# Kernel optimization log

Hardware: AMD Instinct MI355X
Metric: run time of the kernel (lower is better)

Reference implementation:

```python
import jax, jax.numpy as jnp
import numpy as np

R, F, H = 256, 1024, 256  # num_robots, num_frontiers, hidden_dim


def setup_inputs() -> dict:
    key = jax.random.key(0)
    ks = jax.random.split(key, 16)
    sc = 0.05
    return {
        "robot_features": jax.random.normal(ks[0], (R, 4), jnp.float32),
        "frontier_features": jax.random.normal(ks[1], (F, 3), jnp.float32),
        # robot encoder: Linear(4,H) -> ReLU -> Linear(H,H)
        "r_w1": jax.random.normal(ks[2], (4, H), jnp.float32) * sc,
        "r_b1": jnp.zeros((H,), jnp.float32),
        "r_w2": jax.random.normal(ks[3], (H, H), jnp.float32) * sc,
        "r_b2": jnp.zeros((H,), jnp.float32),
        # frontier encoder: Linear(3,H) -> ReLU -> Linear(H,H)
        "f_w1": jax.random.normal(ks[4], (3, H), jnp.float32) * sc,
        "f_b1": jnp.zeros((H,), jnp.float32),
        "f_w2": jax.random.normal(ks[5], (H, H), jnp.float32) * sc,
        "f_b2": jnp.zeros((H,), jnp.float32),
        # affinity predictor: Linear(2H,H) -> ReLU -> Linear(H,1)
        "a_w1": jax.random.normal(ks[6], (2 * H, H), jnp.float32) * sc,
        "a_b1": jnp.zeros((H,), jnp.float32),
        "a_w2": jax.random.normal(ks[7], (H, 1), jnp.float32) * sc,
        "a_b2": jnp.zeros((1,), jnp.float32),
    }


def reference(robot_features, frontier_features,
              r_w1, r_b1, r_w2, r_b2,
              f_w1, f_b1, f_w2, f_b2,
              a_w1, a_b1, a_w2, a_b2):
    # encoders: Linear -> ReLU -> Linear
    robot_embed = jax.nn.relu(robot_features @ r_w1 + r_b1) @ r_w2 + r_b2      # (R, H)
    frontier_embed = jax.nn.relu(frontier_features @ f_w1 + f_b1) @ f_w2 + f_b2  # (F, H)

    # Vectorized pairwise concat: split a_w1 into robot/frontier halves so we
    # never materialize the (R, F, 2H) concat explicitly.
    w1_r, w1_f = a_w1[:robot_embed.shape[1]], a_w1[robot_embed.shape[1]:]
    h = robot_embed @ w1_r  # (R, H)
    h = h[:, None, :] + (frontier_embed @ w1_f)[None, :, :] + a_b1  # (R, F, H)
    h = jax.nn.relu(h)
    affinity = (h @ a_w2)[..., 0] + a_b2[0]  # (R, F)
    return affinity
```

## Files before the change

kernel.cpp:

```cpp
#include <hip/hip_runtime.h>
#include <hip/hip_bf16.h>

#define H 256
#define R_N 256
#define F_N 1024

__global__ __launch_bounds__(256) void embed_kernel(
    const float* __restrict__ rf, const float* __restrict__ ff,
    const float* __restrict__ r_w1, const float* __restrict__ r_b1,
    const float* __restrict__ r_w2, const float* __restrict__ r_b2,
    const float* __restrict__ f_w1, const float* __restrict__ f_b1,
    const float* __restrict__ f_w2, const float* __restrict__ f_b2,
    const float* __restrict__ a_w1, const float* __restrict__ a_b1,
    float* __restrict__ u, float* __restrict__ v)
{
    const int t = threadIdx.x;
    __shared__ float a_s[4][H];
    __shared__ float e_s[4][H];

    if (blockIdx.x < 64) {
        const int r0 = blockIdx.x * 4;
        #pragma unroll
        for (int g = 0; g < 4; ++g) {
            const int r = r0 + g;
            float acc = r_b1[t];
            acc = fmaf(rf[r * 4 + 0], r_w1[0 * H + t], acc);
            acc = fmaf(rf[r * 4 + 1], r_w1[1 * H + t], acc);
            acc = fmaf(rf[r * 4 + 2], r_w1[2 * H + t], acc);
            acc = fmaf(rf[r * 4 + 3], r_w1[3 * H + t], acc);
            a_s[g][t] = fmaxf(acc, 0.0f);
        }
        __syncthreads();

        float e0 = r_b2[t], e1 = e0, e2 = e0, e3 = e0;
        #pragma unroll 8
        for (int k = 0; k < H; ++k) {
            const float w = r_w2[k * H + t];
            e0 = fmaf(a_s[0][k], w, e0);
            e1 = fmaf(a_s[1][k], w, e1);
            e2 = fmaf(a_s[2][k], w, e2);
            e3 = fmaf(a_s[3][k], w, e3);
        }
        __syncthreads();
        e_s[0][t] = e0; e_s[1][t] = e1; e_s[2][t] = e2; e_s[3][t] = e3;
        __syncthreads();

        float u0 = 0.f, u1 = 0.f, u2 = 0.f, u3 = 0.f;
        #pragma unroll 8
        for (int n = 0; n < H; ++n) {
            const float w = a_w1[n * H + t];
            u0 = fmaf(e_s[0][n], w, u0);
            u1 = fmaf(e_s[1][n], w, u1);
            u2 = fmaf(e_s[2][n], w, u2);
            u3 = fmaf(e_s[3][n], w, u3);
        }
        u[(r0 + 0) * H + t] = u0;
        u[(r0 + 1) * H + t] = u1;
        u[(r0 + 2) * H + t] = u2;
        u[(r0 + 3) * H + t] = u3;
    } else {
        const int f0 = (blockIdx.x - 64) * 4;
        #pragma unroll
        for (int g = 0; g < 4; ++g) {
            const int f = f0 + g;
            float acc = f_b1[t];
            acc = fmaf(ff[f * 3 + 0], f_w1[0 * H + t], acc);
            acc = fmaf(ff[f * 3 + 1], f_w1[1 * H + t], acc);
            acc = fmaf(ff[f * 3 + 2], f_w1[2 * H + t], acc);
            a_s[g][t] = fmaxf(acc, 0.0f);
        }
        __syncthreads();

        float e0 = f_b2[t], e1 = e0, e2 = e0, e3 = e0;
        #pragma unroll 8
        for (int k = 0; k < H; ++k) {
            const float w = f_w2[k * H + t];
            e0 = fmaf(a_s[0][k], w, e0);
            e1 = fmaf(a_s[1][k], w, e1);
            e2 = fmaf(a_s[2][k], w, e2);
            e3 = fmaf(a_s[3][k], w, e3);
        }
        __syncthreads();
        e_s[0][t] = e0; e_s[1][t] = e1; e_s[2][t] = e2; e_s[3][t] = e3;
        __syncthreads();

        const float bias = a_b1[t];
        float v0 = bias, v1 = bias, v2 = bias, v3 = bias;
        #pragma unroll 8
        for (int n = 0; n < H; ++n) {
            const float w = a_w1[(H + n) * H + t];
            v0 = fmaf(e_s[0][n], w, v0);
            v1 = fmaf(e_s[1][n], w, v1);
            v2 = fmaf(e_s[2][n], w, v2);
            v3 = fmaf(e_s[3][n], w, v3);
        }
        v[(f0 + 0) * H + t] = v0;
        v[(f0 + 1) * H + t] = v1;
        v[(f0 + 2) * H + t] = v2;
        v[(f0 + 3) * H + t] = v3;
    }
}

#define PAD 260

__global__ __launch_bounds__(256) void affinity_kernel(
    const float* __restrict__ u, const float* __restrict__ v,
    const float* __restrict__ a_w2, const float* __restrict__ a_b2,
    float* __restrict__ out)
{
    __shared__ float u_s[32][PAD];
    __shared__ float v_s[32][PAD];
    __shared__ float w_s[H];

    const int t  = threadIdx.x;
    const int r0 = (blockIdx.x >> 5) * 32;
    const int f0 = (blockIdx.x & 31) * 32;

    w_s[t] = a_w2[t];

    {
        const int rr = t >> 6;
        const int cc = (t & 63) << 2;
        #pragma unroll
        for (int i = 0; i < 8; ++i) {
            const int row = rr + i * 4;
            *(float4*)&u_s[row][cc] = *(const float4*)&u[(r0 + row) * H + cc];
            *(float4*)&v_s[row][cc] = *(const float4*)&v[(f0 + row) * H + cc];
        }
    }
    __syncthreads();

    const int fi = t & 15;
    const int ri = t >> 4;

    float acc00 = 0.f, acc01 = 0.f, acc10 = 0.f, acc11 = 0.f;
    #pragma unroll 4
    for (int k = 0; k < H; k += 4) {
        const float4 w4 = *(const float4*)&w_s[k];
        const float4 ua = *(const float4*)&u_s[ri][k];
        const float4 ub = *(const float4*)&u_s[ri + 16][k];
        const float4 va = *(const float4*)&v_s[fi][k];
        const float4 vb = *(const float4*)&v_s[fi + 16][k];

        acc00 = fmaf(fmaxf(ua.x + va.x, 0.f), w4.x, acc00);
        acc00 = fmaf(fmaxf(ua.y + va.y, 0.f), w4.y, acc00);
        acc00 = fmaf(fmaxf(ua.z + va.z, 0.f), w4.z, acc00);
        acc00 = fmaf(fmaxf(ua.w + va.w, 0.f), w4.w, acc00);

        acc01 = fmaf(fmaxf(ua.x + vb.x, 0.f), w4.x, acc01);
        acc01 = fmaf(fmaxf(ua.y + vb.y, 0.f), w4.y, acc01);
        acc01 = fmaf(fmaxf(ua.z + vb.z, 0.f), w4.z, acc01);
        acc01 = fmaf(fmaxf(ua.w + vb.w, 0.f), w4.w, acc01);

        acc10 = fmaf(fmaxf(ub.x + va.x, 0.f), w4.x, acc10);
        acc10 = fmaf(fmaxf(ub.y + va.y, 0.f), w4.y, acc10);
        acc10 = fmaf(fmaxf(ub.z + va.z, 0.f), w4.z, acc10);
        acc10 = fmaf(fmaxf(ub.w + va.w, 0.f), w4.w, acc10);

        acc11 = fmaf(fmaxf(ub.x + vb.x, 0.f), w4.x, acc11);
        acc11 = fmaf(fmaxf(ub.y + vb.y, 0.f), w4.y, acc11);
        acc11 = fmaf(fmaxf(ub.z + vb.z, 0.f), w4.z, acc11);
        acc11 = fmaf(fmaxf(ub.w + vb.w, 0.f), w4.w, acc11);
    }

    const float b = a_b2[0];
    out[(r0 + ri)      * F_N + f0 + fi]      = acc00 + b;
    out[(r0 + ri)      * F_N + f0 + fi + 16] = acc01 + b;
    out[(r0 + ri + 16) * F_N + f0 + fi]      = acc10 + b;
    out[(r0 + ri + 16) * F_N + f0 + fi + 16] = acc11 + b;
}

extern "C" void kernel_launch(void* const* d_in, const int* in_sizes, int n_in,
                              void* d_out, int out_size, void* d_ws, size_t ws_size,
                              hipStream_t stream) {
    const float* rf   = (const float*)d_in[0];
    const float* ff   = (const float*)d_in[1];
    const float* r_w1 = (const float*)d_in[2];
    const float* r_b1 = (const float*)d_in[3];
    const float* r_w2 = (const float*)d_in[4];
    const float* r_b2 = (const float*)d_in[5];
    const float* f_w1 = (const float*)d_in[6];
    const float* f_b1 = (const float*)d_in[7];
    const float* f_w2 = (const float*)d_in[8];
    const float* f_b2 = (const float*)d_in[9];
    const float* a_w1 = (const float*)d_in[10];
    const float* a_b1 = (const float*)d_in[11];
    const float* a_w2 = (const float*)d_in[12];
    const float* a_b2 = (const float*)d_in[13];

    float* u = (float*)d_ws;
    float* v = u + R_N * H;

    embed_kernel<<<320, 256, 0, stream>>>(rf, ff, r_w1, r_b1, r_w2, r_b2,
                                          f_w1, f_b1, f_w2, f_b2,
                                          a_w1, a_b1, u, v);
    affinity_kernel<<<256, 256, 0, stream>>>(u, v, a_w2, a_b2, (float*)d_out);
}
```

Baseline: 31.03 us.

## Split K across waves in embed and affinity kernels with shared-memory reduction

The embed kernel now handles 8 rows per block (160 blocks instead of 320). Each wave covers a quarter of the K dimension with float4 weight loads and an 8x4 register tile, and partial sums are reduced through shared memory. The affinity kernel moves to 512 threads with a 4-way K split and a 4x2 output tile per thread, then reduces through shared memory. The aim is to cut per-thread serial K loops and raise weight-load reuse, at the cost of extra reduction traffic, more barriers and larger shared-memory footprints.

```diff
diff --git a/kernel.cpp b/kernel.cpp
--- a/kernel.cpp
+++ b/kernel.cpp
@@ -4,6 +4,12 @@
 #define H 256
 #define R_N 256
 #define F_N 1024
+
+#define FMA4(A, s, W) \
+    A.x = fmaf((s), (W).x, A.x); \
+    A.y = fmaf((s), (W).y, A.y); \
+    A.z = fmaf((s), (W).z, A.z); \
+    A.w = fmaf((s), (W).w, A.w);
 
 __global__ __launch_bounds__(256) void embed_kernel(
     const float* __restrict__ rf, const float* __restrict__ ff,
@@ -14,160 +20,206 @@
     const float* __restrict__ a_w1, const float* __restrict__ a_b1,
     float* __restrict__ u, float* __restrict__ v)
 {
-    const int t = threadIdx.x;
-    __shared__ float a_s[4][H];
-    __shared__ float e_s[4][H];
-
-    if (blockIdx.x < 64) {
-        const int r0 = blockIdx.x * 4;
-        #pragma unroll
-        for (int g = 0; g < 4; ++g) {
-            const int r = r0 + g;
-            float acc = r_b1[t];
-            acc = fmaf(rf[r * 4 + 0], r_w1[0 * H + t], acc);
-            acc = fmaf(rf[r * 4 + 1], r_w1[1 * H + t], acc);
-            acc = fmaf(rf[r * 4 + 2], r_w1[2 * H + t], acc);
-            acc = fmaf(rf[r * 4 + 3], r_w1[3 * H + t], acc);
-            a_s[g][t] = fmaxf(acc, 0.0f);
-        }
-        __syncthreads();
-
-        float e0 = r_b2[t], e1 = e0, e2 = e0, e3 = e0;
+    const int t  = threadIdx.x;
+    const int wp = t >> 6;
+    const int c  = (t & 63) * 4;
+
+    __shared__ float aT[H][8];
+    __shared__ float red[4][8][H];
+
+    const bool robot = blockIdx.x < 32;
+    const int  g0    = robot ? blockIdx.x * 8 : (blockIdx.x - 32) * 8;
+
+    const float* __restrict__ x   = robot ? (rf + g0 * 4) : (ff + g0 * 3);
+    const int                 ind = robot ? 4 : 3;
+    const float* __restrict__ w1  = robot ? r_w1 : f_w1;
+    const float* __restrict__ b1  = robot ? r_b1 : f_b1;
+    const float* __restrict__ W2  = robot ? r_w2 : f_w2;
+    const float* __restrict__ b2  = robot ? r_b2 : f_b2;
+    const int                 k3  = robot ? 0 : H;
+    float* __restrict__       dst = robot ? u : v;
+
+    {
+        float l1[8];
+        const float bb = b1[t];
+        #pragma unroll
+        for (int g = 0; g < 8; ++g) {
+            float acc = bb;
+            for (int j = 0; j < ind; ++j)
+                acc = fmaf(x[g * ind + j], w1[j * H + t], acc);
+            l1[g] = fmaxf(acc, 0.0f);
+        }
+        *(float4*)&aT[t][0] = make_float4(l1[0], l1[1], l1[2], l1[3]);
+        *(float4*)&aT[t][4] = make_float4(l1[4], l1[5], l1[6], l1[7]);
+    }
+    __syncthreads();
+
+    {
+        float4 acc[8];
+        #pragma unroll
+        for (int g = 0; g < 8; ++g) acc[g] = make_float4(0.f, 0.f, 0.f, 0.f);
+
+        const int kbase = wp * 64;
         #pragma unroll 8
-        for (int k = 0; k < H; ++k) {
-            const float w = r_w2[k * H + t];
-            e0 = fmaf(a_s[0][k], w, e0);
-            e1 = fmaf(a_s[1][k], w, e1);
-            e2 = fmaf(a_s[2][k], w, e2);
-            e3 = fmaf(a_s[3][k], w, e3);
-        }
-        __syncthreads();
-        e_s[0][t] = e0; e_s[1][t] = e1; e_s[2][t] = e2; e_s[3][t] = e3;
-        __syncthreads();
-
-        float u0 = 0.f, u1 = 0.f, u2 = 0.f, u3 = 0.f;
+        for (int kk = 0; kk < 64; ++kk) {
+            const int k = kbase + kk;
+            const float4 w4  = *(const float4*)&W2[k * H + c];
+            const float4 alo = *(const float4*)&aT[k][0];
+            const float4 ahi = *(const float4*)&aT[k][4];
+            FMA4(acc[0], alo.x, w4); FMA4(acc[1], alo.y, w4);
+            FMA4(acc[2], alo.z, w4); FMA4(acc[3], alo.w, w4);
+            FMA4(acc[4], ahi.x, w4); FMA4(acc[5], ahi.y, w4);
+            FMA4(acc[6], ahi.z, w4); FMA4(acc[7], ahi.w, w4);
+        }
+        #pragma unroll
+        for (int g = 0; g < 8; ++g) *(float4*)&red[wp][g][c] = acc[g];
+    }
+    __syncthreads();
+
+    {
+        float e[8];
+        const float bb = b2[t];
+        #pragma unroll
+        for (int g = 0; g < 8; ++g)
+            e[g] = red[0][g][t] + red[1][g][t] + red[2][g][t] + red[3][g][t] + bb;
+        *(float4*)&aT[t][0] = make_float4(e[0], e[1], e[2], e[3]);
+        *(float4*)&aT[t][4] = make_float4(e[4], e[5], e[6], e[7]);
+    }
+    __syncthreads();
+
+    {
+        float4 acc[8];
+        #pragma unroll
+        for (int g = 0; g < 8; ++g) acc[g] = make_float4(0.f, 0.f, 0.f, 0.f);
+
+        const int kbase = wp * 64;
         #pragma unroll 8
-        for (int n = 0; n < H; ++n) {
-            const float w = a_w1[n * H + t];
-            u0 = fmaf(e_s[0][n], w, u0);
-            u1 = fmaf(e_s[1][n], w, u1);
-            u2 = fmaf(e_s[2][n], w, u2);
-            u3 = fmaf(e_s[3][n], w, u3);
-        }
-        u[(r0 + 0) * H + t] = u0;
-        u[(r0 + 1) * H + t] = u1;
-        u[(r0 + 2) * H + t] = u2;
-        u[(r0 + 3) * H + t] = u3;
-    } else {
-        const int f0 = (blockIdx.x - 64) * 4;
-        #pragma unroll
-        for (int g = 0; g < 4; ++g) {
-            const int f = f0 + g;
-            float acc = f_b1[t];
-            acc = fmaf(ff[f * 3 + 0], f_w1[0 * H + t], acc);
-            acc = fmaf(ff[f * 3 + 1], f_w1[1 * H + t], acc);
-            acc = fmaf(ff[f * 3 + 2], f_w1[2 * H + t], acc);
-            a_s[g][t] = fmaxf(acc, 0.0f);
-        }
-        __syncthreads();
-
-        float e0 = f_b2[t], e1 = e0, e2 = e0, e3 = e0;
-        #pragma unroll 8
-        for (int k = 0; k < H; ++k) {
-            const float w = f_w2[k * H + t];
-            e0 = fmaf(a_s[0][k], w, e0);
-            e1 = fmaf(a_s[1][k], w, e1);
-            e2 = fmaf(a_s[2][k], w, e2);
-            e3 = fmaf(a_s[3][k], w, e3);
-        }
-        __syncthreads();
-        e_s[0][t] = e0; e_s[1][t] = e1; e_s[2][t] = e2; e_s[3][t] = e3;
-        __syncthreads();
-
-        const float bias = a_b1[t];
-        float v0 = bias, v1 = bias, v2 = bias, v3 = bias;
-        #pragma unroll 8
-        for (int n = 0; n < H; ++n) {
-            const float w = a_w1[(H + n) * H + t];
-            v0 = fmaf(e_s[0][n], w, v0);
-            v1 = fmaf(e_s[1][n], w, v1);
-            v2 = fmaf(e_s[2][n], w, v2);
-            v3 = fmaf(e_s[3][n], w, v3);
-        }
-        v[(f0 + 0) * H + t] = v0;
-        v[(f0 + 1) * H + t] = v1;
-        v[(f0 + 2) * H + t] = v2;
-        v[(f0 + 3) * H + t] = v3;
+        for (int kk = 0; kk < 64; ++kk) {
+            const int k = kbase + kk;
+            const float4 w4  = *(const float4*)&a_w1[(k3 + k) * H + c];
+            const float4 alo = *(const float4*)&aT[k][0];
+            const float4 ahi = *(const float4*)&aT[k][4];
+            FMA4(acc[0], alo.x, w4); FMA4(acc[1], alo.y, w4);
+            FMA4(acc[2], alo.z, w4); FMA4(acc[3], alo.w, w4);
+            FMA4(acc[4], ahi.x, w4); FMA4(acc[5], ahi.y, w4);
+            FMA4(acc[6], ahi.z, w4); FMA4(acc[7], ahi.w, w4);
+        }
+        #pragma unroll
+        for (int g = 0; g < 8; ++g) *(float4*)&red[wp][g][c] = acc[g];
+    }
+    __syncthreads();
+
+    {
+        const float ab = robot ? 0.0f : a_b1[t];
+        #pragma unroll
+        for (int g = 0; g < 8; ++g) {
+            const float s = red[0][g][t] + red[1][g][t] + red[2][g][t] + red[3][g][t] + ab;
+            dst[(g0 + g) * H + t] = s;
+        }
     }
 }
 
-#define PAD 260
-
-__global__ __launch_bounds__(256) void affinity_kernel(
+#define LDP 260
+
+__global__ __launch_bounds__(512) void affinity_kernel(
     const float* __restrict__ u, const float* __restrict__ v,
     const float* __restrict__ a_w2, const float* __restrict__ a_b2,
     float* __restrict__ out)
 {
-    __shared__ float u_s[32][PAD];
-    __shared__ float v_s[32][PAD];
+    __shared__ float u_s[32][LDP];
+    __shared__ float v_s[32][LDP];
     __shared__ float w_s[H];
+    __shared__ float red[4][32][33];
 
     const int t  = threadIdx.x;
     const int r0 = (blockIdx.x >> 5) * 32;
     const int f0 = (blockIdx.x & 31) * 32;
 
-    w_s[t] = a_w2[t];
-
-    {
-        const int rr = t >> 6;
-        const int cc = (t & 63) << 2;
-        #pragma unroll
-        for (int i = 0; i < 8; ++i) {
-            const int row = rr + i * 4;
-            *(float4*)&u_s[row][cc] = *(const float4*)&u[(r0 + row) * H + cc];
-            *(float4*)&v_s[row][cc] = *(const float4*)&v[(f0 + row) * H + cc];
-        }
-    }
-    __syncthreads();
-
-    const int fi = t & 15;
-    const int ri = t >> 4;
-
-    float acc00 = 0.f, acc01 = 0.f, acc10 = 0.f, acc11 = 0.f;
+    #pragma unroll
+    for (int i = 0; i < 4; ++i) {
+        const int slot = t + i * 512;
+        const int row  = slot >> 6;
+        const int cc   = (slot & 63) * 4;
+        *(float4*)&u_s[row][cc] = *(const float4*)&u[(r0 + row) * H + cc];
+        *(float4*)&v_s[row][cc] = *(const float4*)&v[(f0 + row) * H + cc];
+    }
+    if (t < 64) *(float4*)&w_s[t * 4] = *(const float4*)&a_w2[t * 4];
+    __syncthreads();
+
+    const int kp = t >> 7;
+    const int t7 = t & 127;
+    const int ri = t7 >> 4;
+    const int fi = t7 & 15;
+    const int k0 = kp * 64;
+
+    float4 accA = make_float4(0.f, 0.f, 0.f, 0.f);
+    float4 accB = make_float4(0.f, 0.f, 0.f, 0.f);
+
     #pragma unroll 4
-    for (int k = 0; k < H; k += 4) {
+    for (int kk = 0; kk < 64; kk += 4) {
+        const int k = k0 + kk;
         const float4 w4 = *(const float4*)&w_s[k];
-        const float4 ua = *(const float4*)&u_s[ri][k];
-        const float4 ub = *(const float4*)&u_s[ri + 16][k];
+        const float4 u0 = *(const float4*)&u_s[ri][k];
+        const float4 u1 = *(const float4*)&u_s[ri +  8][k];
+        const float4 u2 = *(const float4*)&u_s[ri + 16][k];
+        const float4 u3 = *(const float4*)&u_s[ri + 24][k];
         const float4 va = *(const float4*)&v_s[fi][k];
         const float4 vb = *(const float4*)&v_s[fi + 16][k];
 
-        acc00 = fmaf(fmaxf(ua.x + va.x, 0.f), w4.x, acc00);
-        acc00 = fmaf(fmaxf(ua.y + va.y, 0.f), w4.y, acc00);
-        acc00 = fmaf(fmaxf(ua.z + va.z, 0.f), w4.z, acc00);
-        acc00 = fmaf(fmaxf(ua.w + va.w, 0.f), w4.w, acc00);
-
-        acc01 = fmaf(fmaxf(ua.x + vb.x, 0.f), w4.x, acc01);
-        acc01 = fmaf(fmaxf(ua.y + vb.y, 0.f), w4.y, acc01);
-        acc01 = fmaf(fmaxf(ua.z + vb.z, 0.f), w4.z, acc01);
-        acc01 = fmaf(fmaxf(ua.w + vb.w, 0.f), w4.w, acc01);
-
-        acc10 = fmaf(fmaxf(ub.x + va.x, 0.f), w4.x, acc10);
-        acc10 = fmaf(fmaxf(ub.y + va.y, 0.f), w4.y, acc10);
-        acc10 = fmaf(fmaxf(ub.z + va.z, 0.f), w4.z, acc10);
-        acc10 = fmaf(fmaxf(ub.w + va.w, 0.f), w4.w, acc10);
-
-        acc11 = fmaf(fmaxf(ub.x + vb.x, 0.f), w4.x, acc11);
-        acc11 = fmaf(fmaxf(ub.y + vb.y, 0.f), w4.y, acc11);
-        acc11 = fmaf(fmaxf(ub.z + vb.z, 0.f), w4.z, acc11);
-        acc11 = fmaf(fmaxf(ub.w + vb.w, 0.f), w4.w, acc11);
-    }
+        accA.x = fmaf(fmaxf(u0.x + va.x, 0.f), w4.x, accA.x);
+        accA.x = fmaf(fmaxf(u0.y + va.y, 0.f), w4.y, accA.x);
+        accA.x = fmaf(fmaxf(u0.z + va.z, 0.f), w4.z, accA.x);
+        accA.x = fmaf(fmaxf(u0.w + va.w, 0.f), w4.w, accA.x);
+        accA.y = fmaf(fmaxf(u1.x + va.x, 0.f), w4.x, accA.y);
+        accA.y = fmaf(fmaxf(u1.y + va.y, 0.f), w4.y, accA.y);
+        accA.y = fmaf(fmaxf(u1.z + va.z, 0.f), w4.z, accA.y);
+        accA.y = fmaf(fmaxf(u1.w + va.w, 0.f), w4.w, accA.y);
+        accA.z = fmaf(fmaxf(u2.x + va.x, 0.f), w4.x, accA.z);
+        accA.z = fmaf(fmaxf(u2.y + va.y, 0.f), w4.y, accA.z);
+        accA.z = fmaf(fmaxf(u2.z + va.z, 0.f), w4.z, accA.z);
+        accA.z = fmaf(fmaxf(u2.w + va.w, 0.f), w4.w, accA.z);
+        accA.w = fmaf(fmaxf(u3.x + va.x, 0.f), w4.x, accA.w);
+        accA.w = fmaf(fmaxf(u3.y + va.y, 0.f), w4.y, accA.w);
+        accA.w = fmaf(fmaxf(u3.z + va.z, 0.f), w4.z, accA.w);
+        accA.w = fmaf(fmaxf(u3.w + va.w, 0.f), w4.w, accA.w);
+
+        accB.x = fmaf(fmaxf(u0.x + vb.x, 0.f), w4.x, accB.x);
+        accB.x = fmaf(fmaxf(u0.y + vb.y, 0.f), w4.y, accB.x);
+        accB.x = fmaf(fmaxf(u0.z + vb.z, 0.f), w4.z, accB.x);
+        accB.x = fmaf(fmaxf(u0.w + vb.w, 0.f), w4.w, accB.x);
+        accB.y = fmaf(fmaxf(u1.x + vb.x, 0.f), w4.x, accB.y);
+        accB.y = fmaf(fmaxf(u1.y + vb.y, 0.f), w4.y, accB.y);
+        accB.y = fmaf(fmaxf(u1.z + vb.z, 0.f), w4.z, accB.y);
+        accB.y = fmaf(fmaxf(u1.w + vb.w, 0.f), w4.w, accB.y);
+        accB.z = fmaf(fmaxf(u2.x + vb.x, 0.f), w4.x, accB.z);
+        accB.z = fmaf(fmaxf(u2.y + vb.y, 0.f), w4.y, accB.z);
+        accB.z = fmaf(fmaxf(u2.z + vb.z, 0.f), w4.z, accB.z);
+        accB.z = fmaf(fmaxf(u2.w + vb.w, 0.f), w4.w, accB.z);
+        accB.w = fmaf(fmaxf(u3.x + vb.x, 0.f), w4.x, accB.w);
+        accB.w = fmaf(fmaxf(u3.y + vb.y, 0.f), w4.y, accB.w);
+        accB.w = fmaf(fmaxf(u3.z + vb.z, 0.f), w4.z, accB.w);
+        accB.w = fmaf(fmaxf(u3.w + vb.w, 0.f), w4.w, accB.w);
+    }
+
+    red[kp][ri]     [fi]      = accA.x;
+    red[kp][ri +  8][fi]      = accA.y;
+    red[kp][ri + 16][fi]      = accA.z;
+    red[kp][ri + 24][fi]      = accA.w;
+    red[kp][ri]     [fi + 16] = accB.x;
+    red[kp][ri +  8][fi + 16] = accB.y;
+    red[kp][ri + 16][fi + 16] = accB.z;
+    red[kp][ri + 24][fi + 16] = accB.w;
+    __syncthreads();
 
     const float b = a_b2[0];
-    out[(r0 + ri)      * F_N + f0 + fi]      = acc00 + b;
-    out[(r0 + ri)      * F_N + f0 + fi + 16] = acc01 + b;
-    out[(r0 + ri + 16) * F_N + f0 + fi]      = acc10 + b;
-    out[(r0 + ri + 16) * F_N + f0 + fi + 16] = acc11 + b;
+    #pragma unroll
+    for (int j = 0; j < 2; ++j) {
+        const int o = t + j * 512;
+        const int r = o >> 5;
+        const int f = o & 31;
+        const float s = red[0][r][f] + red[1][r][f] + red[2][r][f] + red[3][r][f] + b;
+        out[(r0 + r) * F_N + f0 + f] = s;
+    }
 }
 
 extern "C" void kernel_launch(void* const* d_in, const int* in_sizes, int n_in,
@@ -191,8 +243,8 @@
     float* u = (float*)d_ws;
     float* v = u + R_N * H;
 
-    embed_kernel<<<320, 256, 0, stream>>>(rf, ff, r_w1, r_b1, r_w2, r_b2,
+    embed_kernel<<<160, 256, 0, stream>>>(rf, ff, r_w1, r_b1, r_w2, r_b2,
                                           f_w1, f_b1, f_w2, f_b2,
                                           a_w1, a_b1, u, v);
-    affinity_kernel<<<256, 256, 0, stream>>>(u, v, a_w2, a_b2, (float*)d_out);
+    affinity_kernel<<<256, 512, 0, stream>>>(u, v, a_w2, a_b2, (float*)d_out);
 }
```

Measured after the change: 35.24 us. +13.6%, slower.

## Split affinity K-reduction across four thread groups with 4x2 register tiles

Applied to the files above, without the earlier changes.

The affinity kernel now runs 512 threads per block. Each group of 128 threads handles one quarter of the hidden dimension and computes a 4x2 output micro-tile, and the four partial sums are combined through a shared-memory reduction buffer. The aim is to double the active waves per block, reuse each loaded v vector across more rows, and coalesce the output stores. The cost is an extra shared-memory buffer, an extra barrier, and a reduction pass before the write.

```diff
diff --git a/kernel.cpp b/kernel.cpp
--- a/kernel.cpp
+++ b/kernel.cpp
@@ -101,73 +101,107 @@
     }
 }
 
-#define PAD 260
-
-__global__ __launch_bounds__(256) void affinity_kernel(
+#define LDP 260
+
+__global__ __launch_bounds__(512) void affinity_kernel(
     const float* __restrict__ u, const float* __restrict__ v,
     const float* __restrict__ a_w2, const float* __restrict__ a_b2,
     float* __restrict__ out)
 {
-    __shared__ float u_s[32][PAD];
-    __shared__ float v_s[32][PAD];
+    __shared__ float u_s[32][LDP];
+    __shared__ float v_s[32][LDP];
     __shared__ float w_s[H];
+    __shared__ float red[4][32][33];
 
     const int t  = threadIdx.x;
     const int r0 = (blockIdx.x >> 5) * 32;
     const int f0 = (blockIdx.x & 31) * 32;
 
-    w_s[t] = a_w2[t];
-
-    {
-        const int rr = t >> 6;
-        const int cc = (t & 63) << 2;
-        #pragma unroll
-        for (int i = 0; i < 8; ++i) {
-            const int row = rr + i * 4;
-            *(float4*)&u_s[row][cc] = *(const float4*)&u[(r0 + row) * H + cc];
-            *(float4*)&v_s[row][cc] = *(const float4*)&v[(f0 + row) * H + cc];
-        }
-    }
+    #pragma unroll
+    for (int i = 0; i < 4; ++i) {
+        const int slot = t + i * 512;
+        const int row  = slot >> 6;
+        const int cc   = (slot & 63) * 4;
+        *(float4*)&u_s[row][cc] = *(const float4*)&u[(r0 + row) * H + cc];
+        *(float4*)&v_s[row][cc] = *(const float4*)&v[(f0 + row) * H + cc];
+    }
+    if (t < 64) *(float4*)&w_s[t * 4] = *(const float4*)&a_w2[t * 4];
     __syncthreads();
 
-    const int fi = t & 15;
-    const int ri = t >> 4;
-
-    float acc00 = 0.f, acc01 = 0.f, acc10 = 0.f, acc11 = 0.f;
+    const int kp = t >> 7;
+    const int t7 = t & 127;
+    const int ri = t7 >> 4;
+    const int fi = t7 & 15;
+    const int k0 = kp * 64;
+
+    float4 accA = make_float4(0.f, 0.f, 0.f, 0.f);
+    float4 accB = make_float4(0.f, 0.f, 0.f, 0.f);
+
     #pragma unroll 4
-    for (int k = 0; k < H; k += 4) {
+    for (int kk = 0; kk < 64; kk += 4) {
+        const int k = k0 + kk;
         const float4 w4 = *(const float4*)&w_s[k];
-        const float4 ua = *(const float4*)&u_s[ri][k];
-        const float4 ub = *(const float4*)&u_s[ri + 16][k];
+        const float4 u0 = *(const float4*)&u_s[ri][k];
+        const float4 u1 = *(const float4*)&u_s[ri +  8][k];
+        const float4 u2 = *(const float4*)&u_s[ri + 16][k];
+        const float4 u3 = *(const float4*)&u_s[ri + 24][k];
         const float4 va = *(const float4*)&v_s[fi][k];
         const float4 vb = *(const float4*)&v_s[fi + 16][k];
 
-        acc00 = fmaf(fmaxf(ua.x + va.x, 0.f), w4.x, acc00);
-        acc00 = fmaf(fmaxf(ua.y + va.y, 0.f), w4.y, acc00);
-        acc00 = fmaf(fmaxf(ua.z + va.z, 0.f), w4.z, acc00);
-        acc00 = fmaf(fmaxf(ua.w + va.w, 0.f), w4.w, acc00);
-
-        acc01 = fmaf(fmaxf(ua.x + vb.x, 0.f), w4.x, acc01);
-        acc01 = fmaf(fmaxf(ua.y + vb.y, 0.f), w4.y, acc01);
-        acc01 = fmaf(fmaxf(ua.z + vb.z, 0.f), w4.z, acc01);
-        acc01 = fmaf(fmaxf(ua.w + vb.w, 0.f), w4.w, acc01);
-
-        acc10 = fmaf(fmaxf(ub.x + va.x, 0.f), w4.x, acc10);
-        acc10 = fmaf(fmaxf(ub.y + va.y, 0.f), w4.y, acc10);
-        acc10 = fmaf(fmaxf(ub.z + va.z, 0.f), w4.z, acc10);
-        acc10 = fmaf(fmaxf(ub.w + va.w, 0.f), w4.w, acc10);
-
-        acc11 = fmaf(fmaxf(ub.x + vb.x, 0.f), w4.x, acc11);
-        acc11 = fmaf(fmaxf(ub.y + vb.y, 0.f), w4.y, acc11);
-        acc11 = fmaf(fmaxf(ub.z + vb.z, 0.f), w4.z, acc11);
-        acc11 = fmaf(fmaxf(ub.w + vb.w, 0.f), w4.w, acc11);
-    }
+        accA.x = fmaf(fmaxf(u0.x + va.x, 0.f), w4.x, accA.x);
+        accA.x = fmaf(fmaxf(u0.y + va.y, 0.f), w4.y, accA.x);
+        accA.x = fmaf(fmaxf(u0.z + va.z, 0.f), w4.z, accA.x);
+        accA.x = fmaf(fmaxf(u0.w + va.w, 0.f), w4.w, accA.x);
+        accA.y = fmaf(fmaxf(u1.x + va.x, 0.f), w4.x, accA.y);
+        accA.y = fmaf(fmaxf(u1.y + va.y, 0.f), w4.y, accA.y);
+        accA.y = fmaf(fmaxf(u1.z + va.z, 0.f), w4.z, accA.y);
+        accA.y = fmaf(fmaxf(u1.w + va.w, 0.f), w4.w, accA.y);
+        accA.z = fmaf(fmaxf(u2.x + va.x, 0.f), w4.x, accA.z);
+        accA.z = fmaf(fmaxf(u2.y + va.y, 0.f), w4.y, accA.z);
+        accA.z = fmaf(fmaxf(u2.z + va.z, 0.f), w4.z, accA.z);
+        accA.z = fmaf(fmaxf(u2.w + va.w, 0.f), w4.w, accA.z);
+        accA.w = fmaf(fmaxf(u3.x + va.x, 0.f), w4.x, accA.w);
+        accA.w = fmaf(fmaxf(u3.y + va.y, 0.f), w4.y, accA.w);
+        accA.w = fmaf(fmaxf(u3.z + va.z, 0.f), w4.z, accA.w);
+        accA.w = fmaf(fmaxf(u3.w + va.w, 0.f), w4.w, accA.w);
+
+        accB.x = fmaf(fmaxf(u0.x + vb.x, 0.f), w4.x, accB.x);
+        accB.x = fmaf(fmaxf(u0.y + vb.y, 0.f), w4.y, accB.x);
+        accB.x = fmaf(fmaxf(u0.z + vb.z, 0.f), w4.z, accB.x);
+        accB.x = fmaf(fmaxf(u0.w + vb.w, 0.f), w4.w, accB.x);
+        accB.y = fmaf(fmaxf(u1.x + vb.x, 0.f), w4.x, accB.y);
+        accB.y = fmaf(fmaxf(u1.y + vb.y, 0.f), w4.y, accB.y);
+        accB.y = fmaf(fmaxf(u1.z + vb.z, 0.f), w4.z, accB.y);
+        accB.y = fmaf(fmaxf(u1.w + vb.w, 0.f), w4.w, accB.y);
+        accB.z = fmaf(fmaxf(u2.x + vb.x, 0.f), w4.x, accB.z);
+        accB.z = fmaf(fmaxf(u2.y + vb.y, 0.f), w4.y, accB.z);
+        accB.z = fmaf(fmaxf(u2.z + vb.z, 0.f), w4.z, accB.z);
+        accB.z = fmaf(fmaxf(u2.w + vb.w, 0.f), w4.w, accB.z);
+        accB.w = fmaf(fmaxf(u3.x + vb.x, 0.f), w4.x, accB.w);
+        accB.w = fmaf(fmaxf(u3.y + vb.y, 0.f), w4.y, accB.w);
+        accB.w = fmaf(fmaxf(u3.z + vb.z, 0.f), w4.z, accB.w);
+        accB.w = fmaf(fmaxf(u3.w + vb.w, 0.f), w4.w, accB.w);
+    }
+
+    red[kp][ri]     [fi]      = accA.x;
+    red[kp][ri +  8][fi]      = accA.y;
+    red[kp][ri + 16][fi]      = accA.z;
+    red[kp][ri + 24][fi]      = accA.w;
+    red[kp][ri]     [fi + 16] = accB.x;
+    red[kp][ri +  8][fi + 16] = accB.y;
+    red[kp][ri + 16][fi + 16] = accB.z;
+    red[kp][ri + 24][fi + 16] = accB.w;
+    __syncthreads();
 
     const float b = a_b2[0];
-    out[(r0 + ri)      * F_N + f0 + fi]      = acc00 + b;
-    out[(r0 + ri)      * F_N + f0 + fi + 16] = acc01 + b;
-    out[(r0 + ri + 16) * F_N + f0 + fi]      = acc10 + b;
-    out[(r0 + ri + 16) * F_N + f0 + fi + 16] = acc11 + b;
+    #pragma unroll
+    for (int j = 0; j < 2; ++j) {
+        const int o = t + j * 512;
+        const int r = o >> 5;
+        const int f = o & 31;
+        const float s = red[0][r][f] + red[1][r][f] + red[2][r][f] + red[3][r][f] + b;
+        out[(r0 + r) * F_N + f0 + f] = s;
+    }
 }
 
 extern "C" void kernel_launch(void* const* d_in, const int* in_sizes, int n_in,
@@ -194,5 +228,5 @@
     embed_kernel<<<320, 256, 0, stream>>>(rf, ff, r_w1, r_b1, r_w2, r_b2,
                                           f_w1, f_b1, f_w2, f_b2,
                                           a_w1, a_b1, u, v);
-    affinity_kernel<<<256, 256, 0, stream>>>(u, v, a_w2, a_b2, (float*)d_out);
+    affinity_kernel<<<256, 512, 0, stream>>>(u, v, a_w2, a_b2, (float*)d_out);
 }
```

Result: faster. 29.61 us (-4.6%).
